# Kernel optimization log

Measured on AMD Instinct MI355X. Metric: run time of the kernel, lower is better.

Reference implementation:

```python
import jax, jax.numpy as jnp
import numpy as np

# decade-bucketed relative risk table from estimate_risk(age): index = age // 10, clipped to 8 (80+)
RISK_TABLE = jnp.array([1.0, 1.0, 0.91, 1.12, 1.71, 2.41, 3.27, 5.18, 8.44], dtype=jnp.float32)


def _swish(x, beta):
    # Swish module: x * sigmoid(beta * x), beta learnable
    return x * jax.nn.sigmoid(beta * x)


def _cox(h, survtime, censor):
    # Cox negative partial log-likelihood (standard loss_fn[0] in survival repos)
    at_risk = survtime[None, :] >= survtime[:, None]  # [B,B]
    log_risk = jax.scipy.special.logsumexp(jnp.where(at_risk, h[None, :], -jnp.inf), axis=1)
    return -jnp.mean((h - log_risk) * censor)


def _pair_rank_loss(h, age, grade, age_thr, grade_mask, beta):
    # vectorized form of hggloss/lggloss: pairs (i<j) with age[i]<thr<=age[j]
    # and both grades in the allowed set; term = log(1 + exp(alpha*(h_i - h_j)))
    B = h.shape[0]
    risk = RISK_TABLE[jnp.clip(age // 10, 0, 8)]  # [B]
    tri = jnp.triu(jnp.ones((B, B), dtype=bool), k=1)
    mask = (tri
            & (age[:, None] < age_thr) & (age[None, :] >= age_thr)
            & grade_mask[:, None] & grade_mask[None, :])
    alpha = _swish((risk[None, :] - risk[:, None]) / 8.0, beta)  # [B,B]
    term = jax.nn.softplus(alpha * (h[:, None] - h[None, :]))    # log(1+exp(.)), stable
    n = jnp.sum(mask)
    total = jnp.sum(jnp.where(mask, term, 0.0))
    return jnp.where(n > 0, total / jnp.maximum(n, 1).astype(h.dtype), jnp.asarray(0.0, h.dtype))


def setup_inputs() -> dict:
    B = 4096
    key = jax.random.key(0)
    k1, k2, k3, k4, k5, k6 = jax.random.split(key, 6)
    return {
        "hazard3d": jax.random.normal(k1, (B,), dtype=jnp.float32),
        "hazard1d": jax.random.normal(k2, (B,), dtype=jnp.float32),
        "survtime": jax.random.uniform(k3, (B,), dtype=jnp.float32),
        "censor": jax.random.randint(k4, (B,), 0, 2).astype(jnp.float32),
        "vars_": jnp.ones((4,), dtype=jnp.float32),
        "beta1": jnp.asarray(1.0, dtype=jnp.float32),
        "beta2": jnp.asarray(1.0, dtype=jnp.float32),
        "age": jax.random.randint(k5, (B,), 0, 100, dtype=jnp.int32),
        "grade": jax.random.randint(k6, (B,), 0, 3, dtype=jnp.int32),
    }


def reference(hazard3d, hazard1d, survtime, censor, vars_, beta1, beta2, age, grade):
    loss3d = _cox(hazard3d, survtime, censor)
    loss1d = _cox(hazard1d, survtime, censor)
    lgg = _pair_rank_loss(hazard3d, age, grade, 40, grade == 0, beta1)
    hgg = _pair_rank_loss(hazard3d, age, grade, 65, (grade == 1) | (grade == 2), beta2)
    losscli = lgg + hgg
    lossd_1 = 0.5 * loss3d / vars_[0] ** 2 + jnp.log(vars_[0])
    lossd_1d_1 = 0.5 * loss1d / vars_[2] ** 2 + jnp.log(vars_[2])
    losscli_1 = 0.5 * losscli / vars_[3] ** 2 + jnp.log(vars_[3])
    return lossd_1 + lossd_1d_1 + losscli_1
```

## Files before the change

kernel.cpp:

```cpp
#include <hip/hip_runtime.h>
#include <math.h>

#define TPB 1024
#define NBUK 4096
#define NPL 20
#define NPH 74
#define NSLOT (2 + NPL + NPH)
#define FLAG_MAGIC 0x13579BDFu

struct Slot {
  double a, b;
  unsigned int c, d;
  unsigned int flag;
  unsigned int pad;
};

__device__ const float RISK[9] = {1.0f, 1.0f, 0.91f, 1.12f, 1.71f,
                                  2.41f, 3.27f, 5.18f, 8.44f};

__device__ __forceinline__ int bucketOf(float s) {
  int b = (int)(s * 4096.0f);
  return b < 0 ? 0 : (b > 4095 ? 4095 : b);
}
__device__ __forceinline__ int decadeOf(int a) {
  int d = a / 10;
  return d > 8 ? 8 : (d < 0 ? 0 : d);
}
__device__ __forceinline__ double wredsumd(double v) {
  for (int off = 32; off; off >>= 1) v += __shfl_down(v, off, 64);
  return v;
}
__device__ __forceinline__ unsigned int wredsumu(unsigned int v) {
  for (int off = 32; off; off >>= 1) v += __shfl_down(v, off, 64);
  return v;
}

__global__ __launch_bounds__(TPB) void fused_kernel(
    const float* __restrict__ h3, const float* __restrict__ h1,
    const float* __restrict__ st, const float* __restrict__ cen,
    const int* __restrict__ age, const int* __restrict__ grade,
    const float* __restrict__ b1p, const float* __restrict__ b2p,
    const float* __restrict__ vars, Slot* __restrict__ slots,
    float* __restrict__ out, int B) {
  __shared__ int smem_i[18432];
  __shared__ int wsi[16];
  __shared__ float wsA[16];
  __shared__ double dred[32];
  __shared__ unsigned int ured[16];

  const int t = threadIdx.x, lane = t & 63, wid = t >> 6;
  const int bid = blockIdx.x;

  if (bid < 2) {
    const float* h = (bid == 0) ? h3 : h1;
    int* cursor = smem_i;
    unsigned short* ord = (unsigned short*)(smem_i + 4096);
    float* bs = (float*)(smem_i + 6144);
    float* h_lds = (float*)(smem_i + 10240);
    float* st_lds = (float*)(smem_i + 14336);

    float s4[4], hv4[4];
    ((int4*)cursor)[t] = make_int4(0, 0, 0, 0);
    if (4 * t + 3 < B) {
      float4 hv = ((const float4*)h)[t];
      float4 sv = ((const float4*)st)[t];
      ((float4*)h_lds)[t] = hv;
      ((float4*)st_lds)[t] = sv;
      hv4[0] = hv.x; hv4[1] = hv.y; hv4[2] = hv.z; hv4[3] = hv.w;
      s4[0] = sv.x; s4[1] = sv.y; s4[2] = sv.z; s4[3] = sv.w;
    } else {
      for (int k = 0; k < 4; ++k) {
        int i = 4 * t + k;
        float hh = (i < B) ? h[i] : 0.f;
        float ss = (i < B) ? st[i] : 2.f;
        h_lds[i] = hh;
        st_lds[i] = ss;
        hv4[k] = hh;
        s4[k] = ss;
      }
    }
    __syncthreads();
    int myb[4];
    for (int k = 0; k < 4; ++k) {
      int i = 4 * t + k;
      int b = (i < B) ? bucketOf(s4[k]) : -1;
      myb[k] = b;
      if (b >= 0) atomicAdd(&cursor[b], 1);
    }
    __syncthreads();
    int c0 = cursor[4 * t], c1 = cursor[4 * t + 1], c2 = cursor[4 * t + 2],
        c3 = cursor[4 * t + 3];
    int loc = c0 + c1 + c2 + c3;
    int v = loc;
    for (int off = 1; off < 64; off <<= 1) {
      int u = __shfl_up(v, off, 64);
      if (lane >= off) v += u;
    }
    if (lane == 63) wsi[wid] = v;
    __syncthreads();
    if (t == 0) {
      int run = 0;
      for (int w = 0; w < 16; ++w) { int x = wsi[w]; wsi[w] = run; run += x; }
    }
    __syncthreads();
    int excl = v - loc + wsi[wid];
    cursor[4 * t + 0] = excl;
    cursor[4 * t + 1] = excl + c0;
    cursor[4 * t + 2] = excl + c0 + c1;
    cursor[4 * t + 3] = excl + c0 + c1 + c2;
    __syncthreads();
    for (int k = 0; k < 4; ++k)
      if (myb[k] >= 0) {
        int slot = atomicAdd(&cursor[myb[k]], 1);
        ord[slot] = (unsigned short)(4 * t + k);
      }
    __syncthreads();
    float pv[4];
    for (int k = 0; k < 4; ++k) {
      int bb = 4 * t + k;
      int lo_ = bb ? cursor[bb - 1] : 0;
      int hi_ = cursor[bb];
      float s = 0.f;
      for (int m = lo_; m < hi_; ++m) s += __expf(h_lds[ord[m]]);
      pv[k] = s;
    }
    float l3 = pv[3], l2 = pv[2] + l3, l1 = pv[1] + l2, l0 = pv[0] + l1;
    float vA = l0;
    for (int off = 1; off < 64; off <<= 1) {
      float u = __shfl_down(vA, off, 64);
      if (lane + off < 64) vA += u;
    }
    if (lane == 0) wsA[wid] = vA;
    __syncthreads();
    if (t == 0) {
      float r = 0.f;
      for (int w = 15; w >= 0; --w) { float x = wsA[w]; wsA[w] = r; r += x; }
    }
    __syncthreads();
    float tail = (vA - l0) + wsA[wid];
    bs[4 * t + 0] = l0 + tail;
    bs[4 * t + 1] = l1 + tail;
    bs[4 * t + 2] = l2 + tail;
    bs[4 * t + 3] = l3 + tail;
    __syncthreads();
    double a = 0.0;
    for (int k = 0; k < 4; ++k) {
      int i = 4 * t + k;
      if (i >= B) break;
      float ci = cen[i];
      if (ci == 0.f) continue;
      float si = s4[k];
      int b = myb[k];
      float T = (b + 1 < NBUK) ? bs[b + 1] : 0.f;
      int lo_ = b ? cursor[b - 1] : 0;
      int hi_ = cursor[b];
      for (int m = lo_; m < hi_; ++m) {
        int j = ord[m];
        if (st_lds[j] >= si) T += __expf(h_lds[j]);
      }
      a += (double)((hv4[k] - __logf(T)) * ci);
    }
    double w = wredsumd(a);
    if (lane == 0) dred[wid] = w;
    __syncthreads();
    if (t == 0) {
      double S = 0;
      for (int w2 = 0; w2 < 16; ++w2) S += dred[w2];
      slots[bid].a = (bid == 0) ? S : 0.0;
      slots[bid].b = (bid == 0) ? 0.0 : S;
      slots[bid].c = 0u;
      slots[bid].d = 0u;
      __hip_atomic_store(&slots[bid].flag, FLAG_MAGIC, __ATOMIC_RELEASE,
                         __HIP_MEMORY_SCOPE_AGENT);
    }
  } else {
    const bool isL = (bid < 2 + NPL);
    const int pb = isL ? (bid - 2) : (bid - 2 - NPL);
    const int NP = isL ? NPL : NPH;
    uint2* pool = (uint2*)smem_i;
    float* aLUT = (float*)(smem_i + 8192);
    int* cnts = (int*)(aLUT + 81);
    const float beta = isL ? b1p[0] : b2p[0];
    const int athr = isL ? 40 : 65;

    if (t < 81) {
      int dy = t / 9, dq = t - 9 * dy;
      float d = (RISK[dq] - RISK[dy]) * 0.125f;
      aLUT[t] = d / (1.f + __expf(-beta * d));
    }
    if (t < 4) cnts[t] = 0;
    __syncthreads();
    int av4[4], cat[4];
    if (4 * t + 3 < B) {
      int4 av = ((const int4*)age)[t];
      int4 gv = ((const int4*)grade)[t];
      av4[0] = av.x; av4[1] = av.y; av4[2] = av.z; av4[3] = av.w;
      int gv4[4] = {gv.x, gv.y, gv.z, gv.w};
      for (int k = 0; k < 4; ++k) {
        bool ok = isL ? (gv4[k] == 0) : (gv4[k] == 1 || gv4[k] == 2);
        cat[k] = ok ? (av4[k] < athr ? 0 : 1) : -1;
      }
    } else {
      for (int k = 0; k < 4; ++k) {
        int i = 4 * t + k;
        cat[k] = -1;
        av4[k] = 0;
        if (i < B) {
          int g = grade[i];
          av4[k] = age[i];
          bool ok = isL ? (g == 0) : (g == 1 || g == 2);
          if (ok) cat[k] = (av4[k] < athr) ? 0 : 1;
        }
      }
    }
    for (int k = 0; k < 4; ++k)
      if (cat[k] >= 0) atomicAdd(&cnts[cat[k]], 1);
    __syncthreads();
    const int ny = cnts[0], no = cnts[1];
    if (t == 0) { cnts[2] = 0; cnts[3] = ny; }
    __syncthreads();
    for (int k = 0; k < 4; ++k) {
      int c = cat[k];
      if (c >= 0) {
        int i = 4 * t + k;
        int slot = atomicAdd(&cnts[2 + c], 1);
        pool[slot] = make_uint2(__float_as_uint(h3[i]),
                                (unsigned)((i << 4) | decadeOf(av4[k])));
      }
    }
    __syncthreads();

    double tot = 0.0;
    unsigned int n = 0;
    for (int yi = pb; yi < ny; yi += NP) {
      uint2 yr = pool[yi];
      float h3y = __uint_as_float(yr.x);
      int iy = (int)(yr.y >> 4);
      const float* aRow = &aLUT[(yr.y & 15u) * 9];
      for (int oi = t; oi < no; oi += TPB) {
        uint2 orc = pool[ny + oi];
        if ((int)(orc.y >> 4) > iy) {
          float x = aRow[orc.y & 15u] * (h3y - __uint_as_float(orc.x));
          float sp = fmaxf(x, 0.f) + __logf(1.f + __expf(-fabsf(x)));
          tot += (double)sp;
          n++;
        }
      }
    }
    double wt = wredsumd(tot);
    unsigned int un = wredsumu(n);
    if (lane == 0) { dred[wid] = wt; ured[wid] = un; }
    __syncthreads();
    if (t == 0) {
      double S = 0;
      unsigned int N = 0;
      for (int w = 0; w < 16; ++w) { S += dred[w]; N += ured[w]; }
      slots[bid].a = isL ? S : 0.0;
      slots[bid].b = isL ? 0.0 : S;
      slots[bid].c = isL ? N : 0u;
      slots[bid].d = isL ? 0u : N;
      __hip_atomic_store(&slots[bid].flag, FLAG_MAGIC, __ATOMIC_RELEASE,
                         __HIP_MEMORY_SCOPE_AGENT);
    }
  }

  if (bid == 0 && wid == 0) {
    double s3 = 0, s1 = 0, tl = 0, th = 0;
    unsigned long long nl = 0, nh = 0;
    for (int s = lane; s < NSLOT; s += 64) {
      while (__hip_atomic_load(&slots[s].flag, __ATOMIC_ACQUIRE,
                               __HIP_MEMORY_SCOPE_AGENT) != FLAG_MAGIC)
        __builtin_amdgcn_s_sleep(8);
      double a = slots[s].a;
      double b = slots[s].b;
      unsigned int c = slots[s].c;
      unsigned int d = slots[s].d;
      if (s < 2) {
        s3 += a;
        s1 += b;
      } else {
        tl += a;
        th += b;
        nl += c;
        nh += d;
      }
    }
    for (int off = 32; off; off >>= 1) {
      s3 += __shfl_down(s3, off, 64);
      s1 += __shfl_down(s1, off, 64);
      tl += __shfl_down(tl, off, 64);
      th += __shfl_down(th, off, 64);
      nl += __shfl_down(nl, off, 64);
      nh += __shfl_down(nh, off, 64);
    }
    if (lane == 0) {
      float loss3d = (float)(-s3 / (double)B);
      float loss1d = (float)(-s1 / (double)B);
      float lgg = nl ? (float)(tl / (double)nl) : 0.f;
      float hgg = nh ? (float)(th / (double)nh) : 0.f;
      float losscli = lgg + hgg;
      float v0 = vars[0], v2 = vars[2], v3 = vars[3];
      float r = 0.5f * loss3d / (v0 * v0) + logf(v0);
      r += 0.5f * loss1d / (v2 * v2) + logf(v2);
      r += 0.5f * losscli / (v3 * v3) + logf(v3);
      out[0] = r;
    }
  }
}

extern "C" void kernel_launch(void* const* d_in, const int* in_sizes, int n_in,
                              void* d_out, int out_size, void* d_ws,
                              size_t ws_size, hipStream_t stream) {
  const float* h3 = (const float*)d_in[0];
  const float* h1 = (const float*)d_in[1];
  const float* st = (const float*)d_in[2];
  const float* cen = (const float*)d_in[3];
  const float* vars = (const float*)d_in[4];
  const float* beta1 = (const float*)d_in[5];
  const float* beta2 = (const float*)d_in[6];
  const int* age = (const int*)d_in[7];
  const int* grade = (const int*)d_in[8];
  const int B = in_sizes[0];

  Slot* slots = (Slot*)d_ws;
  float* out = (float*)d_out;

  fused_kernel<<<NSLOT, TPB, 0, stream>>>(h3, h1, st, cen, age, grade, beta1,
                                          beta2, vars, slots, out, B);
}
```

Before: 82.20 us.

## Replace LDS atomics with ballot-based compaction and move final reducer block

In the pair-rank blocks, the shared-memory atomic counters used to split records into young and old pools are replaced by wave ballots, popcounts and a per-wave prefix, which removes one barrier and the atomic contention. h3 and censor values are now loaded once as vectors up front instead of being re-read per element. The final cross-block reduction moves from block 0 to the last block, and its spin-wait sleep is shortened. Pool ordering changes from atomic order to deterministic index order, which should not alter the result.

```diff
diff --git a/kernel.cpp b/kernel.cpp
--- a/kernel.cpp
+++ b/kernel.cpp
@@ -59,15 +59,17 @@
     float* h_lds = (float*)(smem_i + 10240);
     float* st_lds = (float*)(smem_i + 14336);
 
-    float s4[4], hv4[4];
+    float s4[4], hv4[4], c4[4];
     ((int4*)cursor)[t] = make_int4(0, 0, 0, 0);
     if (4 * t + 3 < B) {
       float4 hv = ((const float4*)h)[t];
       float4 sv = ((const float4*)st)[t];
+      float4 cv = ((const float4*)cen)[t];
       ((float4*)h_lds)[t] = hv;
       ((float4*)st_lds)[t] = sv;
       hv4[0] = hv.x; hv4[1] = hv.y; hv4[2] = hv.z; hv4[3] = hv.w;
       s4[0] = sv.x; s4[1] = sv.y; s4[2] = sv.z; s4[3] = sv.w;
+      c4[0] = cv.x; c4[1] = cv.y; c4[2] = cv.z; c4[3] = cv.w;
     } else {
       for (int k = 0; k < 4; ++k) {
         int i = 4 * t + k;
@@ -77,6 +79,7 @@
         st_lds[i] = ss;
         hv4[k] = hh;
         s4[k] = ss;
+        c4[k] = (i < B) ? cen[i] : 0.f;
       }
     }
     __syncthreads();
@@ -147,7 +150,7 @@
     for (int k = 0; k < 4; ++k) {
       int i = 4 * t + k;
       if (i >= B) break;
-      float ci = cen[i];
+      float ci = c4[k];
       if (ci == 0.f) continue;
       float si = s4[k];
       int b = myb[k];
@@ -179,7 +182,8 @@
     const int NP = isL ? NPL : NPH;
     uint2* pool = (uint2*)smem_i;
     float* aLUT = (float*)(smem_i + 8192);
-    int* cnts = (int*)(aLUT + 81);
+    int* wcY = (int*)(aLUT + 81);
+    int* wcO = wcY + 16;
     const float beta = isL ? b1p[0] : b2p[0];
     const int athr = isL ? 40 : 65;
 
@@ -188,13 +192,14 @@
       float d = (RISK[dq] - RISK[dy]) * 0.125f;
       aLUT[t] = d / (1.f + __expf(-beta * d));
     }
-    if (t < 4) cnts[t] = 0;
-    __syncthreads();
     int av4[4], cat[4];
+    float hv4[4];
     if (4 * t + 3 < B) {
       int4 av = ((const int4*)age)[t];
       int4 gv = ((const int4*)grade)[t];
+      float4 hv = ((const float4*)h3)[t];
       av4[0] = av.x; av4[1] = av.y; av4[2] = av.z; av4[3] = av.w;
+      hv4[0] = hv.x; hv4[1] = hv.y; hv4[2] = hv.z; hv4[3] = hv.w;
       int gv4[4] = {gv.x, gv.y, gv.z, gv.w};
       for (int k = 0; k < 4; ++k) {
         bool ok = isL ? (gv4[k] == 0) : (gv4[k] == 1 || gv4[k] == 2);
@@ -205,28 +210,47 @@
         int i = 4 * t + k;
         cat[k] = -1;
         av4[k] = 0;
+        hv4[k] = 0.f;
         if (i < B) {
           int g = grade[i];
           av4[k] = age[i];
+          hv4[k] = h3[i];
           bool ok = isL ? (g == 0) : (g == 1 || g == 2);
           if (ok) cat[k] = (av4[k] < athr) ? 0 : 1;
         }
       }
     }
-    for (int k = 0; k < 4; ++k)
-      if (cat[k] >= 0) atomicAdd(&cnts[cat[k]], 1);
-    __syncthreads();
-    const int ny = cnts[0], no = cnts[1];
-    if (t == 0) { cnts[2] = 0; cnts[3] = ny; }
-    __syncthreads();
-    for (int k = 0; k < 4; ++k) {
-      int c = cat[k];
-      if (c >= 0) {
+    unsigned long long mY[4], mO[4];
+    int yc = 0, oc = 0;
+    for (int k = 0; k < 4; ++k) {
+      mY[k] = __ballot(cat[k] == 0);
+      mO[k] = __ballot(cat[k] == 1);
+      yc += __popcll(mY[k]);
+      oc += __popcll(mO[k]);
+    }
+    if (lane == 0) { wcY[wid] = yc; wcO[wid] = oc; }
+    __syncthreads();
+    int ny = 0, no = 0, bY = 0, bO = 0;
+    for (int w = 0; w < 16; ++w) {
+      int y = wcY[w], o = wcO[w];
+      if (w < wid) { bY += y; bO += o; }
+      ny += y;
+      no += o;
+    }
+    const unsigned long long lt = (1ull << lane) - 1ull;
+    int offY = 0, offO = 0;
+    for (int k = 0; k < 4; ++k) {
+      if (cat[k] >= 0) {
         int i = 4 * t + k;
-        int slot = atomicAdd(&cnts[2 + c], 1);
-        pool[slot] = make_uint2(__float_as_uint(h3[i]),
-                                (unsigned)((i << 4) | decadeOf(av4[k])));
-      }
+        uint2 rec = make_uint2(__float_as_uint(hv4[k]),
+                               (unsigned)((i << 4) | decadeOf(av4[k])));
+        int slot = (cat[k] == 0)
+                       ? (bY + offY + __popcll(mY[k] & lt))
+                       : (ny + bO + offO + __popcll(mO[k] & lt));
+        pool[slot] = rec;
+      }
+      offY += __popcll(mY[k]);
+      offO += __popcll(mO[k]);
     }
     __syncthreads();
 
@@ -264,13 +288,13 @@
     }
   }
 
-  if (bid == 0 && wid == 0) {
+  if (bid == NSLOT - 1 && wid == 0) {
     double s3 = 0, s1 = 0, tl = 0, th = 0;
     unsigned long long nl = 0, nh = 0;
     for (int s = lane; s < NSLOT; s += 64) {
       while (__hip_atomic_load(&slots[s].flag, __ATOMIC_ACQUIRE,
                                __HIP_MEMORY_SCOPE_AGENT) != FLAG_MAGIC)
-        __builtin_amdgcn_s_sleep(8);
+        __builtin_amdgcn_s_sleep(2);
       double a = slots[s].a;
       double b = slots[s].b;
       unsigned int c = slots[s].c;
```

Result: no change. 82.52 us (+0.4%).
